# Kernel tuning notes

Measured on AMD Instinct MI355X. Metric: run time of the kernel, lower is better.

Reference implementation:

```python
import jax, jax.numpy as jnp
import numpy as np

B, S, D = 2, 2048, 1024
H, KVH, HD = 16, 1, 64
E, K, HID = 8, 2, 4096
EPS = 1e-5


def rmsnorm(x, scale):
    ms = jnp.mean(x * x, axis=-1, keepdims=True)
    return x * jax.lax.rsqrt(ms + EPS) * scale


def setup_inputs() -> dict:
    key = jax.random.key(0)
    ks = jax.random.split(key, 12)
    s = lambda k, shape, fan: jax.random.normal(k, shape, jnp.float32) * (fan ** -0.5)
    return {
        "x": jax.random.normal(ks[0], (B, S, D), jnp.float32),
        "g_pre_mqa": jnp.ones((D,), jnp.float32),
        "g_post_mqa": jnp.ones((D,), jnp.float32),
        "g_pre_moe": jnp.ones((D,), jnp.float32),
        "g_post_moe": jnp.ones((D,), jnp.float32),
        "Wq": s(ks[1], (D, H * HD), D),
        "Wk": s(ks[2], (D, KVH * HD), D),
        "Wv": s(ks[3], (D, KVH * HD), D),
        "Wo": s(ks[4], (H * HD, D), H * HD),
        "Wg": s(ks[5], (D, E), D),
        "We1": s(ks[6], (E, D, HID), D),
        "We2": s(ks[7], (E, HID, D), HID),
    }


def mqa(x, Wq, Wk, Wv, Wo):
    b, s, _ = x.shape
    q = (x @ Wq).reshape(b, s, H, HD).transpose(0, 2, 1, 3)     # [B,H,S,hd]
    k = (x @ Wk).reshape(b, s, KVH, HD).transpose(0, 2, 1, 3)   # [B,1,S,hd]
    v = (x @ Wv).reshape(b, s, KVH, HD).transpose(0, 2, 1, 3)
    scores = jnp.einsum('bhqd,bhkd->bhqk', q, jnp.broadcast_to(k, (b, H, s, HD))) / np.sqrt(HD)
    probs = jax.nn.softmax(scores, axis=-1)  # note: no causal mask, matching _standard_attention
    out = jnp.einsum('bhqk,bhkd->bhqd', probs, jnp.broadcast_to(v, (b, H, s, HD)))
    out = out.transpose(0, 2, 1, 3).reshape(b, s, H * HD)
    return out @ Wo


def moe(h, Wg, We1, We2):
    logits = h @ Wg                       # [B,S,E]
    probs = jax.nn.softmax(logits, axis=-1)
    topv, topi = jax.lax.top_k(probs, K)  # [B,S,K]
    # scatter top-k probs into full expert vector (non-chosen experts -> 0)
    routing = jnp.sum(jax.nn.one_hot(topi, E, dtype=h.dtype) * topv[..., None], axis=-2)  # [B,S,E]
    mid = jax.nn.gelu(jnp.einsum('bsd,edh->bseh', h, We1))
    eo = jnp.einsum('bseh,ehd->bsed', mid, We2)
    out = jnp.einsum('bse,bsed->bsd', routing, eo)
    return out, probs


def reference(x, g_pre_mqa, g_post_mqa, g_pre_moe, g_post_moe, Wq, Wk, Wv, Wo, Wg, We1, We2):
    # inference path: dropout and router noise disabled (training=False)
    x = x + rmsnorm(mqa(rmsnorm(x, g_pre_mqa), Wq, Wk, Wv, Wo), g_post_mqa)
    moe_out, routing_probs = moe(rmsnorm(x, g_pre_moe), Wg, We1, We2)
    x = x + rmsnorm(moe_out, g_post_moe)
    return x, routing_probs
```

## Files before the change

kernel.cpp:

```cpp
#include <hip/hip_runtime.h>
#include <hip/hip_bf16.h>
#include <math.h>

#define NTOK   4096
#define DMODEL 1024
#define SEQL   2048
#define QKVW   1152
#define NH     16
#define HDIM   64
#define NE     8
#define HIDD   4096
#define EPSV   1e-5f
#define KT     32

#define ASCL   256.f
#define WSCL   4096.f
#define OUTSCL (1.f/1048576.f)
#define SSCALE (0.125f/65536.f)
#define PBIAS  10.397207708399179f
#define DTHR   0.5f

typedef __attribute__((ext_vector_type(8))) short bf16x8;
typedef __attribute__((ext_vector_type(8))) _Float16 f16x8;
typedef __attribute__((ext_vector_type(4))) _Float16 f16x4;
typedef __attribute__((ext_vector_type(4))) float f32x4;

#define GLOBAL_AS __attribute__((address_space(1)))
#define LDS_AS    __attribute__((address_space(3)))
__device__ __forceinline__ void gl_lds16(const void* g, void* l){
  __builtin_amdgcn_global_load_lds((const GLOBAL_AS void*)g, (LDS_AS void*)l, 16u, 0, 0u);
}

__device__ __forceinline__ short f2b(float x){
  __hip_bfloat16 h = __float2bfloat16(x);
  return *reinterpret_cast<short*>(&h);
}
__device__ __forceinline__ void split2h(float x, _Float16& a, _Float16& b){
  a = (_Float16)x;
  b = (_Float16)(x - (float)a);
}

__global__ __launch_bounds__(256) void transpose_conv_kernel(
    const float* __restrict__ in, short* __restrict__ out,
    int R, int C, long inb, long outb)
{
  __shared__ float tile[32][33];
  in  += (size_t)blockIdx.z * inb;
  out += (size_t)blockIdx.z * outb;
  int c0 = blockIdx.x*32, r0 = blockIdx.y*32;
  int tx = threadIdx.x & 31, ty = threadIdx.x >> 5;
  #pragma unroll
  for (int i=0;i<4;i++)
    tile[ty+i*8][tx] = in[(size_t)(r0+ty+i*8)*C + c0+tx];
  __syncthreads();
  int cl = threadIdx.x >> 3, quad = threadIdx.x & 7;
  short4 s;
  s.x = f2b(tile[quad*4+0][cl]);
  s.y = f2b(tile[quad*4+1][cl]);
  s.z = f2b(tile[quad*4+2][cl]);
  s.w = f2b(tile[quad*4+3][cl]);
  *(short4*)&out[(size_t)(c0+cl)*R + r0 + quad*4] = s;
}

__global__ __launch_bounds__(256) void transpose_split2f16_kernel(
    const float* __restrict__ in, _Float16* __restrict__ o1, _Float16* __restrict__ o2,
    int R, int C, int rowOff, int outLD)
{
  __shared__ float tile[32][33];
  int c0 = blockIdx.x*32, r0 = blockIdx.y*32;
  int tx = threadIdx.x & 31, ty = threadIdx.x >> 5;
  #pragma unroll
  for (int i=0;i<4;i++)
    tile[ty+i*8][tx] = in[(size_t)(r0+ty+i*8)*C + c0+tx];
  __syncthreads();
  #pragma unroll
  for (int i=0;i<4;i++){
    float v = tile[tx][ty+i*8] * WSCL;
    _Float16 va,vb; split2h(v,va,vb);
    size_t idx = (size_t)(c0+ty+i*8+rowOff)*outLD + r0+tx;
    o1[idx]=va; o2[idx]=vb;
  }
}

__global__ __launch_bounds__(256) void rms_split2_kernel(
    const float* __restrict__ x, const float* __restrict__ g,
    _Float16* __restrict__ o1, _Float16* __restrict__ o2)
{
  int row = blockIdx.x, tid = threadIdx.x;
  const float4* xr = (const float4*)(x + (size_t)row*DMODEL);
  float4 v = xr[tid];
  float ss = v.x*v.x + v.y*v.y + v.z*v.z + v.w*v.w;
  #pragma unroll
  for (int off=32; off; off>>=1) ss += __shfl_down(ss, off);
  __shared__ float red[4];
  if ((tid&63)==0) red[tid>>6] = ss;
  __syncthreads();
  float rs = rsqrtf((red[0]+red[1]+red[2]+red[3])*(1.f/1024.f) + EPSV) * ASCL;
  float4 gv = ((const float4*)g)[tid];
  float o[4] = {v.x*rs*gv.x, v.y*rs*gv.y, v.z*rs*gv.z, v.w*rs*gv.w};
  f16x4 s1,s2;
  #pragma unroll
  for (int c=0;c<4;c++){ _Float16 a,b; split2h(o[c],a,b); s1[c]=a; s2[c]=b; }
  size_t base = (size_t)row*DMODEL + tid*4;
  *(f16x4*)(o1+base) = s1; *(f16x4*)(o2+base) = s2;
}

__global__ __launch_bounds__(256) void vtrans_split2_kernel(
    const _Float16* __restrict__ p1, const _Float16* __restrict__ p2,
    _Float16* __restrict__ o1, _Float16* __restrict__ o2)
{
  __shared__ float tile[32][33];
  int s0 = blockIdx.x*32, d0 = blockIdx.y*32, bb = blockIdx.z;
  int tx = threadIdx.x & 31, ty = threadIdx.x >> 5;
  #pragma unroll
  for (int i=0;i<4;i++){
    size_t idx = (size_t)(bb*SEQL + s0+ty+i*8)*QKVW + DMODEL+HDIM + d0+tx;
    tile[ty+i*8][tx] = (float)p1[idx] + (float)p2[idx];
  }
  __syncthreads();
  #pragma unroll
  for (int i=0;i<4;i++){
    float v = tile[tx][ty+i*8];
    _Float16 va,vb; split2h(v,va,vb);
    size_t idx = (size_t)(bb*HDIM + d0+ty+i*8)*SEQL + s0+tx;
    o1[idx]=va; o2[idx]=vb;
  }
}

__global__ __launch_bounds__(256) void gemm_f16x2_kernel(
    const _Float16* __restrict__ a1, const _Float16* __restrict__ a2,
    const _Float16* __restrict__ b1, const _Float16* __restrict__ b2,
    float* __restrict__ C, int K, int ldc, float outscale)
{
  __shared__ _Float16 lsA[2][128*32];
  __shared__ _Float16 lsB[2][128*32];
  int m0 = blockIdx.y*128, n0 = blockIdx.x*128;
  int tid = threadIdx.x, wave = tid>>6, lane = tid&63;
  int g = lane>>4, li = lane&15;
  int wm = (wave>>1)*64, wn = (wave&1)*64;
  const _Float16* Ap[2] = {a1,a2};
  const _Float16* Bp[2] = {b1,b2};
  int srow = wave*32 + (lane>>2), scol = (lane&3)*8;
  const _Float16* gA[2][2]; const _Float16* gB[2][2];
  #pragma unroll
  for (int p=0;p<2;p++)
    #pragma unroll
    for (int i=0;i<2;i++){
      gA[p][i] = Ap[p] + (size_t)(m0+srow+i*16)*K + scol;
      gB[p][i] = Bp[p] + (size_t)(n0+srow+i*16)*K + scol;
    }
  f32x4 acc[4][4] = {};
  for (int k0=0; k0<K; k0+=32){
    #pragma unroll
    for (int p=0;p<2;p++)
      #pragma unroll
      for (int i=0;i<2;i++){
        gl_lds16(gA[p][i]+k0, &lsA[p][(wave*32+i*16)*32]);
        gl_lds16(gB[p][i]+k0, &lsB[p][(wave*32+i*16)*32]);
      }
    __syncthreads();
    #pragma unroll
    for (int i=0;i<2;i++){
      f16x8 af[4];
      #pragma unroll
      for (int m=0;m<4;m++) af[m] = *(f16x8*)&lsA[i][(wm+m*16+li)*32 + g*8];
      #pragma unroll
      for (int j=0;j<2-i;j++){
        #pragma unroll
        for (int n=0;n<4;n++){
          f16x8 bfr = *(f16x8*)&lsB[j][(wn+n*16+li)*32 + g*8];
          #pragma unroll
          for (int m=0;m<4;m++)
            acc[m][n] = __builtin_amdgcn_mfma_f32_16x16x32_f16(af[m], bfr, acc[m][n], 0,0,0);
        }
      }
    }
    __syncthreads();
  }
  #pragma unroll
  for (int m=0;m<4;m++){
    int lr0 = wm + m*16 + g*4;
    #pragma unroll
    for (int n=0;n<4;n++){
      int col = n0 + wn + n*16 + li;
      #pragma unroll
      for (int r=0;r<4;r++)
        C[(size_t)(m0+lr0+r)*ldc + col] = acc[m][n][r]*outscale;
    }
  }
}

__global__ __launch_bounds__(256) void gemm_f16x2s_kernel(
    const _Float16* __restrict__ a1, const _Float16* __restrict__ a2,
    const _Float16* __restrict__ b1, const _Float16* __restrict__ b2,
    _Float16* __restrict__ o1, _Float16* __restrict__ o2, int K, int ldc, float outscale)
{
  __shared__ _Float16 lsA[2][128*32];
  __shared__ _Float16 lsB[2][128*32];
  int m0 = blockIdx.y*128, n0 = blockIdx.x*128;
  int tid = threadIdx.x, wave = tid>>6, lane = tid&63;
  int g = lane>>4, li = lane&15;
  int wm = (wave>>1)*64, wn = (wave&1)*64;
  const _Float16* Ap[2] = {a1,a2};
  const _Float16* Bp[2] = {b1,b2};
  int srow = wave*32 + (lane>>2), scol = (lane&3)*8;
  const _Float16* gA[2][2]; const _Float16* gB[2][2];
  #pragma unroll
  for (int p=0;p<2;p++)
    #pragma unroll
    for (int i=0;i<2;i++){
      gA[p][i] = Ap[p] + (size_t)(m0+srow+i*16)*K + scol;
      gB[p][i] = Bp[p] + (size_t)(n0+srow+i*16)*K + scol;
    }
  f32x4 acc[4][4] = {};
  for (int k0=0; k0<K; k0+=32){
    #pragma unroll
    for (int p=0;p<2;p++)
      #pragma unroll
      for (int i=0;i<2;i++){
        gl_lds16(gA[p][i]+k0, &lsA[p][(wave*32+i*16)*32]);
        gl_lds16(gB[p][i]+k0, &lsB[p][(wave*32+i*16)*32]);
      }
    __syncthreads();
    #pragma unroll
    for (int i=0;i<2;i++){
      f16x8 af[4];
      #pragma unroll
      for (int m=0;m<4;m++) af[m] = *(f16x8*)&lsA[i][(wm+m*16+li)*32 + g*8];
      #pragma unroll
      for (int j=0;j<2-i;j++){
        #pragma unroll
        for (int n=0;n<4;n++){
          f16x8 bfr = *(f16x8*)&lsB[j][(wn+n*16+li)*32 + g*8];
          #pragma unroll
          for (int m=0;m<4;m++)
            acc[m][n] = __builtin_amdgcn_mfma_f32_16x16x32_f16(af[m], bfr, acc[m][n], 0,0,0);
        }
      }
    }
    __syncthreads();
  }
  #pragma unroll
  for (int m=0;m<4;m++){
    int lr0 = wm + m*16 + g*4;
    #pragma unroll
    for (int n=0;n<4;n++){
      int col = n0 + wn + n*16 + li;
      #pragma unroll
      for (int r=0;r<4;r++){
        float val = acc[m][n][r]*outscale;
        _Float16 xa,xb; split2h(val,xa,xb);
        size_t idx = (size_t)(m0+lr0+r)*ldc + col;
        o1[idx]=xa; o2[idx]=xb;
      }
    }
  }
}

__global__ __launch_bounds__(256) void attn_f16_kernel(
    const _Float16* __restrict__ q1, const _Float16* __restrict__ q2,
    const _Float16* __restrict__ v1, const _Float16* __restrict__ v2,
    _Float16* __restrict__ o1, _Float16* __restrict__ o2)
{
  __shared__ _Float16 Ks[32*136];
  __shared__ _Float16 Vs[64*72];
  int qt = blockIdx.x, h = blockIdx.y, b = blockIdx.z;
  int tid = threadIdx.x, wave = tid>>6, lane = tid&63;
  int g = lane>>4, li = lane&15;
  size_t qbase = (size_t)b*SEQL + qt*128;
  const _Float16* qsrc[2] = {q1,q2};
  const _Float16* vsrc[2] = {v1,v2};
  f16x8 qf[2][2][2];
  #pragma unroll
  for (int nf=0;nf<2;nf++){
    size_t qrow = qbase + wave*32 + nf*16 + li;
    #pragma unroll
    for (int j=0;j<2;j++)
      #pragma unroll
      for (int kk=0;kk<2;kk++)
        qf[nf][j][kk] = *(const f16x8*)(qsrc[j] + qrow*QKVW + h*HDIM + kk*32 + g*8);
  }
  const _Float16* kga[2]; int klds[2];
  const _Float16* vga[2]; int vlds[2];
  #pragma unroll
  for (int i=0;i<2;i++){
    int c = tid + 256*i;
    { int row=c>>4, sub=c&15, pl=sub>>3, d=(sub&7)*8;
      kga[i] = qsrc[pl] + ((size_t)b*SEQL + row)*QKVW + DMODEL + d;
      klds[i] = row*136 + pl*64 + d; }
    { int row=c>>3, sub=c&7, pl=sub>>2, s8=(sub&3)*8;
      vga[i] = vsrc[pl] + ((size_t)b*HDIM + row)*SEQL + s8;
      vlds[i] = row*72 + pl*32 + s8; }
  }
  f16x8 kreg[2], vreg[2];
  #pragma unroll
  for (int i=0;i<2;i++){ kreg[i]=*(const f16x8*)kga[i]; vreg[i]=*(const f16x8*)vga[i]; }

  float m_run[2] = {-1e30f,-1e30f}, l_run[2] = {0.f,0.f};
  f32x4 acc_o[4][2] = {};
  int src1 = (((2*g)&3)<<4) + li;
  int src2 = (((2*g+1)&3)<<4) + li;
  bool hi_half = (g>=2);

  for (int kvt=0; kvt<SEQL/KT; kvt++){
    #pragma unroll
    for (int i=0;i<2;i++){
      *(f16x8*)&Ks[klds[i]] = kreg[i];
      *(f16x8*)&Vs[vlds[i]] = vreg[i];
    }
    __syncthreads();
    if (kvt+1 < SEQL/KT){
      #pragma unroll
      for (int i=0;i<2;i++){
        kreg[i] = *(const f16x8*)(kga[i] + (size_t)(kvt+1)*KT*QKVW);
        vreg[i] = *(const f16x8*)(vga[i] + (size_t)(kvt+1)*KT);
      }
    }
    f32x4 s_acc[2][2] = {};
    __builtin_amdgcn_s_setprio(1);
    #pragma unroll
    for (int i=0;i<2;i++){
      #pragma unroll
      for (int kk=0;kk<2;kk++){
        f16x8 af[2];
        #pragma unroll
        for (int mf=0;mf<2;mf++)
          af[mf] = *(f16x8*)&Ks[(mf*16+li)*136 + i*64 + kk*32 + g*8];
        #pragma unroll
        for (int j=0;j<2-i;j++){
          #pragma unroll
          for (int nf=0;nf<2;nf++){
            #pragma unroll
            for (int mf=0;mf<2;mf++)
              s_acc[mf][nf] = __builtin_amdgcn_mfma_f32_16x16x32_f16(af[mf], qf[nf][j][kk], s_acc[mf][nf], 0,0,0);
          }
        }
      }
    }
    __builtin_amdgcn_s_setprio(0);
    float p[2][2][4];
    #pragma unroll
    for (int nf=0;nf<2;nf++){
      float mx = -1e30f;
      #pragma unroll
      for (int mf=0;mf<2;mf++)
        #pragma unroll
        for (int r=0;r<4;r++) mx = fmaxf(mx, s_acc[mf][nf][r]);
      mx = fmaxf(mx, __shfl_xor(mx,16));
      mx = fmaxf(mx, __shfl_xor(mx,32));
      mx *= SSCALE;
      if (!__all(mx <= m_run[nf] + DTHR)){
        float mn = fmaxf(m_run[nf], mx);
        float al = __expf(m_run[nf] - mn);
        m_run[nf] = mn;
        l_run[nf] *= al;
        #pragma unroll
        for (int mfd=0; mfd<4; mfd++){
          acc_o[mfd][nf][0]*=al; acc_o[mfd][nf][1]*=al;
          acc_o[mfd][nf][2]*=al; acc_o[mfd][nf][3]*=al;
        }
      }
      float rsum = 0.f;
      #pragma unroll
      for (int mf=0;mf<2;mf++)
        #pragma unroll
        for (int r=0;r<4;r++){
          float pv = __expf(s_acc[mf][nf][r]*SSCALE - m_run[nf] + PBIAS);
          p[mf][nf][r] = pv; rsum += pv;
        }
      rsum += __shfl_xor(rsum,16);
      rsum += __shfl_xor(rsum,32);
      l_run[nf] += rsum;
    }
    f16x8 fp_frag[2][2];
    #pragma unroll
    for (int nf=0;nf<2;nf++){
      float p8[8];
      #pragma unroll
      for (int jj=0;jj<4;jj++){
        float v0 = __shfl(p[0][nf][jj], src1);
        float vv1 = __shfl(p[1][nf][jj], src1);
        p8[jj] = hi_half ? vv1 : v0;
        float w0 = __shfl(p[0][nf][jj], src2);
        float w1 = __shfl(p[1][nf][jj], src2);
        p8[4+jj] = hi_half ? w1 : w0;
      }
      #pragma unroll
      for (int jj=0;jj<8;jj++){
        _Float16 xa,xb; split2h(p8[jj], xa,xb);
        fp_frag[nf][0][jj]=xa; fp_frag[nf][1][jj]=xb;
      }
    }
    __builtin_amdgcn_s_setprio(1);
    #pragma unroll
    for (int vj=0;vj<2;vj++){
      f16x8 av[4];
      #pragma unroll
      for (int mfd=0;mfd<4;mfd++)
        av[mfd] = *(f16x8*)&Vs[(mfd*16+li)*72 + vj*32 + g*8];
      #pragma unroll
      for (int pi=0; pi<2-vj; pi++)
        #pragma unroll
        for (int mfd=0;mfd<4;mfd++)
          #pragma unroll
          for (int nf=0;nf<2;nf++)
            acc_o[mfd][nf] = __builtin_amdgcn_mfma_f32_16x16x32_f16(av[mfd], fp_frag[nf][pi], acc_o[mfd][nf], 0,0,0);
    }
    __builtin_amdgcn_s_setprio(0);
    __syncthreads();
  }
  #pragma unroll
  for (int nf=0;nf<2;nf++){
    float inv = 1.f/l_run[nf];
    size_t q = qbase + wave*32 + nf*16 + li;
    #pragma unroll
    for (int mfd=0;mfd<4;mfd++){
      int d0 = mfd*16 + g*4;
      f16x4 sa,sb;
      #pragma unroll
      for (int r=0;r<4;r++){
        _Float16 xa,xb; split2h(acc_o[mfd][nf][r]*inv, xa,xb);
        sa[r]=xa; sb[r]=xb;
      }
      size_t base = q*DMODEL + h*HDIM + d0;
      *(f16x4*)(o1+base)=sa; *(f16x4*)(o2+base)=sb;
    }
  }
}

__global__ __launch_bounds__(256) void attnres_router_kernel(
    const float* __restrict__ x, const float* __restrict__ ao,
    const float* __restrict__ gpost, const float* __restrict__ gpre,
    const float* __restrict__ Wg,
    float* __restrict__ x2, short* __restrict__ h,
    float* __restrict__ probs_out, int* __restrict__ tok_list,
    float* __restrict__ w_list, int* __restrict__ counts)
{
  int row = blockIdx.x, tid = threadIdx.x;
  float4 a  = ((const float4*)(ao + (size_t)row*DMODEL))[tid];
  float4 xv = ((const float4*)(x  + (size_t)row*DMODEL))[tid];
  float ss = a.x*a.x + a.y*a.y + a.z*a.z + a.w*a.w;
  #pragma unroll
  for (int off=32; off; off>>=1) ss += __shfl_down(ss, off);
  __shared__ float red[4];
  if ((tid&63)==0) red[tid>>6] = ss;
  __syncthreads();
  float rs1 = rsqrtf((red[0]+red[1]+red[2]+red[3])*(1.f/1024.f) + EPSV);
  float4 gp = ((const float4*)gpost)[tid];
  float4 o;
  o.x = xv.x + a.x*rs1*gp.x; o.y = xv.y + a.y*rs1*gp.y;
  o.z = xv.z + a.z*rs1*gp.z; o.w = xv.w + a.w*rs1*gp.w;
  ((float4*)(x2 + (size_t)row*DMODEL))[tid] = o;
  float s2 = o.x*o.x + o.y*o.y + o.z*o.z + o.w*o.w;
  __syncthreads();
  #pragma unroll
  for (int off=32; off; off>>=1) s2 += __shfl_down(s2, off);
  if ((tid&63)==0) red[tid>>6] = s2;
  __syncthreads();
  float rs2 = rsqrtf((red[0]+red[1]+red[2]+red[3])*(1.f/1024.f) + EPSV);
  float4 gm = ((const float4*)gpre)[tid];
  float n0 = o.x*rs2*gm.x, n1 = o.y*rs2*gm.y, n2 = o.z*rs2*gm.z, n3 = o.w*rs2*gm.w;
  short4 hs;
  hs.x = f2b(n0); hs.y = f2b(n1); hs.z = f2b(n2); hs.w = f2b(n3);
  *(short4*)(h + (size_t)row*DMODEL + tid*4) = hs;
  const float* wr = Wg + (size_t)(tid*4)*NE;
  float le[8];
  #pragma unroll
  for (int e=0;e<8;e++)
    le[e] = n0*wr[e] + n1*wr[NE+e] + n2*wr[2*NE+e] + n3*wr[3*NE+e];
  #pragma unroll
  for (int e=0;e<8;e++)
    #pragma unroll
    for (int off=32; off; off>>=1) le[e] += __shfl_xor(le[e], off);
  __shared__ float redl[4][8];
  if ((tid&63)==0)
    #pragma unroll
    for (int e=0;e<8;e++) redl[tid>>6][e] = le[e];
  __syncthreads();
  if (tid == 0){
    float l[8];
    #pragma unroll
    for (int e=0;e<8;e++) l[e] = redl[0][e]+redl[1][e]+redl[2][e]+redl[3][e];
    float mx = l[0];
    #pragma unroll
    for (int e=1;e<8;e++) mx = fmaxf(mx, l[e]);
    float pp[8], s = 0.f;
    #pragma unroll
    for (int e=0;e<8;e++){ pp[e] = expf(l[e]-mx); s += pp[e]; }
    float inv = 1.f/s;
    #pragma unroll
    for (int e=0;e<8;e++){ pp[e] *= inv; probs_out[(size_t)row*NE + e] = pp[e]; }
    int i1 = 0;
    #pragma unroll
    for (int e=1;e<8;e++) if (pp[e] > pp[i1]) i1 = e;
    int i2 = (i1==0) ? 1 : 0;
    #pragma unroll
    for (int e=0;e<8;e++) if (e != i1 && pp[e] > pp[i2]) i2 = e;
    int pos = atomicAdd(&counts[i1], 1);
    tok_list[i1*NTOK+pos] = row;
    w_list[i1*NTOK+pos] = pp[i1];
    pos = atomicAdd(&counts[i2], 1);
    tok_list[i2*NTOK+pos] = row | (1<<16);
    w_list[i2*NTOK+pos] = pp[i2];
  }
}

__global__ __launch_bounds__(256) void moe_gemm1_kernel(
    const short* __restrict__ h, const short* __restrict__ we1t,
    const int* __restrict__ tok_list, const int* __restrict__ counts,
    short* __restrict__ mid)
{
  int e = blockIdx.z;
  int cnt = counts[e];
  int m0 = blockIdx.y*128, n0 = blockIdx.x*128;
  if (m0 >= cnt) return;
  int base = 0;
  for (int j=0;j<NE;j++){ int c = counts[j]; if (j<e) base += c; }
  const short* Bt = we1t + (size_t)e*HIDD*DMODEL;
  const int* tl = tok_list + e*NTOK;
  __shared__ short lsA[128*32];
  __shared__ short lsB[128*32];
  int tid = threadIdx.x, wave = tid>>6, lane = tid&63;
  int li = lane&15, g = lane>>4;
  int wm = (wave>>1)*64, wn = (wave&1)*64;
  int srow = wave*32 + (lane>>2), scol = (lane&3)*8;
  const short* gA[2]; const short* gB[2];
  #pragma unroll
  for (int i=0;i<2;i++){
    int rr = min(m0+srow+i*16, cnt-1);
    gA[i] = h + (size_t)(tl[rr] & 0xFFFF)*DMODEL + scol;
    gB[i] = Bt + (size_t)(n0+srow+i*16)*DMODEL + scol;
  }
  f32x4 acc[4][4] = {};
  for (int k0=0; k0<DMODEL; k0+=32){
    #pragma unroll
    for (int i=0;i<2;i++){
      gl_lds16(gA[i]+k0, &lsA[(wave*32+i*16)*32]);
      gl_lds16(gB[i]+k0, &lsB[(wave*32+i*16)*32]);
    }
    __syncthreads();
    bf16x8 af[4], bfr[4];
    #pragma unroll
    for (int m=0;m<4;m++) af[m] = *(bf16x8*)&lsA[(wm+m*16+li)*32 + g*8];
    #pragma unroll
    for (int n=0;n<4;n++) bfr[n] = *(bf16x8*)&lsB[(wn+n*16+li)*32 + g*8];
    #pragma unroll
    for (int m=0;m<4;m++)
      #pragma unroll
      for (int n=0;n<4;n++)
        acc[m][n] = __builtin_amdgcn_mfma_f32_16x16x32_bf16(af[m], bfr[n], acc[m][n], 0,0,0);
    __syncthreads();
  }
  #pragma unroll
  for (int m=0;m<4;m++){
    int lr0 = wm + m*16 + (g<<2);
    #pragma unroll
    for (int n=0;n<4;n++){
      int col = n0 + wn + n*16 + li;
      #pragma unroll
      for (int r=0;r<4;r++){
        int gr = m0 + lr0 + r;
        if (gr < cnt){
          float tval = acc[m][n][r];
          float u = 1.5957691216057308f*(tval + 0.044715f*tval*tval*tval);
          float ge = tval / (1.f + __expf(-u));
          mid[(size_t)(base+gr)*HIDD + col] = f2b(ge);
        }
      }
    }
  }
}

__global__ __launch_bounds__(256) void moe_gemm2_kernel(
    const short* __restrict__ mid, const short* __restrict__ we2t,
    const int* __restrict__ tok_list, const float* __restrict__ w_list,
    const int* __restrict__ counts, float* __restrict__ eo)
{
  int e = blockIdx.z;
  int cnt = counts[e];
  int m0 = blockIdx.y*128, n0 = blockIdx.x*128;
  if (m0 >= cnt) return;
  int base = 0;
  for (int j=0;j<NE;j++){ int c = counts[j]; if (j<e) base += c; }
  const short* A  = mid + (size_t)base*HIDD;
  const short* Bt = we2t + (size_t)e*DMODEL*HIDD;
  const int* tl = tok_list + e*NTOK;
  const float* wl = w_list + e*NTOK;
  __shared__ short lsA[128*32];
  __shared__ short lsB[128*32];
  int tid = threadIdx.x, wave = tid>>6, lane = tid&63;
  int li = lane&15, g = lane>>4;
  int wm = (wave>>1)*64, wn = (wave&1)*64;
  int srow = wave*32 + (lane>>2), scol = (lane&3)*8;
  const short* gA[2]; const short* gB[2];
  #pragma unroll
  for (int i=0;i<2;i++){
    int rr = min(m0+srow+i*16, cnt-1);
    gA[i] = A + (size_t)rr*HIDD + scol;
    gB[i] = Bt + (size_t)(n0+srow+i*16)*HIDD + scol;
  }
  f32x4 acc[4][4] = {};
  for (int k0=0; k0<HIDD; k0+=32){
    #pragma unroll
    for (int i=0;i<2;i++){
      gl_lds16(gA[i]+k0, &lsA[(wave*32+i*16)*32]);
      gl_lds16(gB[i]+k0, &lsB[(wave*32+i*16)*32]);
    }
    __syncthreads();
    bf16x8 af[4], bfr[4];
    #pragma unroll
    for (int m=0;m<4;m++) af[m] = *(bf16x8*)&lsA[(wm+m*16+li)*32 + g*8];
    #pragma unroll
    for (int n=0;n<4;n++) bfr[n] = *(bf16x8*)&lsB[(wn+n*16+li)*32 + g*8];
    #pragma unroll
    for (int m=0;m<4;m++)
      #pragma unroll
      for (int n=0;n<4;n++)
        acc[m][n] = __builtin_amdgcn_mfma_f32_16x16x32_bf16(af[m], bfr[n], acc[m][n], 0,0,0);
    __syncthreads();
  }
  #pragma unroll
  for (int m=0;m<4;m++){
    int lr0 = wm + m*16 + (g<<2);
    #pragma unroll
    for (int n=0;n<4;n++){
      int col = n0 + wn + n*16 + li;
      #pragma unroll
      for (int r=0;r<4;r++){
        int gr = m0 + lr0 + r;
        if (gr < cnt){
          int pv = tl[gr];
          eo[((size_t)(pv>>16)*NTOK + (pv & 0xFFFF))*DMODEL + col] = wl[gr]*acc[m][n][r];
        }
      }
    }
  }
}

__global__ __launch_bounds__(256) void final_kernel(
    const float* __restrict__ x2, const float* __restrict__ eo,
    const float* __restrict__ g, float* __restrict__ out)
{
  int row = blockIdx.x, tid = threadIdx.x;
  float4 m0 = ((const float4*)(eo + (size_t)row*DMODEL))[tid];
  float4 m1 = ((const float4*)(eo + (size_t)(NTOK+row)*DMODEL))[tid];
  float4 mv;
  mv.x = m0.x+m1.x; mv.y = m0.y+m1.y; mv.z = m0.z+m1.z; mv.w = m0.w+m1.w;
  float4 xv = ((const float4*)(x2  + (size_t)row*DMODEL))[tid];
  float ss = mv.x*mv.x + mv.y*mv.y + mv.z*mv.z + mv.w*mv.w;
  #pragma unroll
  for (int off=32; off; off>>=1) ss += __shfl_down(ss, off);
  __shared__ float red[4];
  if ((tid&63)==0) red[tid>>6] = ss;
  __syncthreads();
  float rs = rsqrtf((red[0]+red[1]+red[2]+red[3])*(1.f/1024.f) + EPSV);
  float4 gv = ((const float4*)g)[tid];
  float4 o;
  o.x = xv.x + mv.x*rs*gv.x; o.y = xv.y + mv.y*rs*gv.y;
  o.z = xv.z + mv.z*rs*gv.z; o.w = xv.w + mv.w*rs*gv.w;
  ((float4*)(out + (size_t)row*DMODEL))[tid] = o;
}

extern "C" void kernel_launch(void* const* d_in, const int* in_sizes, int n_in,
                              void* d_out, int out_size, void* d_ws, size_t ws_size,
                              hipStream_t stream) {
  (void)in_sizes; (void)n_in; (void)out_size; (void)ws_size;
  const float* x          = (const float*)d_in[0];
  const float* g_pre_mqa  = (const float*)d_in[1];
  const float* g_post_mqa = (const float*)d_in[2];
  const float* g_pre_moe  = (const float*)d_in[3];
  const float* g_post_moe = (const float*)d_in[4];
  const float* Wq         = (const float*)d_in[5];
  const float* Wk         = (const float*)d_in[6];
  const float* Wv         = (const float*)d_in[7];
  const float* Wo         = (const float*)d_in[8];
  const float* Wg         = (const float*)d_in[9];
  const float* We1        = (const float*)d_in[10];
  const float* We2        = (const float*)d_in[11];

  float* out_x = (float*)d_out;
  float* out_probs = out_x + (size_t)NTOK*DMODEL;

  char* p = (char*)d_ws;
  size_t off = 0;
  auto alloc = [&](size_t bytes)->char*{
    char* r = p + off; off = (off + bytes + 255) & ~(size_t)255; return r; };

  short* we1t = (short*)alloc((size_t)NE*HIDD*DMODEL*2);
  short* we2t = (short*)alloc((size_t)NE*DMODEL*HIDD*2);
  short* mid  = (short*)alloc((size_t)2*NTOK*HIDD*2);

  char* regA = alloc((size_t)2*NTOK*DMODEL*2);
  _Float16* xn1p1 = (_Float16*)regA;
  _Float16* xn1p2 = (_Float16*)(regA + (size_t)NTOK*DMODEL*2);
  float* ao       = (float*)regA;

  _Float16* wqkvT1 = (_Float16*)alloc((size_t)QKVW*DMODEL*2);
  _Float16* wqkvT2 = (_Float16*)alloc((size_t)QKVW*DMODEL*2);
  _Float16* woT1   = (_Float16*)alloc((size_t)DMODEL*DMODEL*2);
  _Float16* woT2   = (_Float16*)alloc((size_t)DMODEL*DMODEL*2);

  char* regB = alloc((size_t)2*NTOK*DMODEL*2);
  _Float16* attnp1 = (_Float16*)regB;
  _Float16* attnp2 = (_Float16*)(regB + (size_t)NTOK*DMODEL*2);

  char* regC = alloc((size_t)2*NTOK*DMODEL*4 + (size_t)NTOK*DMODEL*2);
  _Float16* qkvf1 = (_Float16*)regC;
  _Float16* qkvf2 = (_Float16*)(regC + (size_t)NTOK*QKVW*2);
  float* eo    = (float*)regC;
  short* hbuf  = (short*)(regC + (size_t)2*NTOK*DMODEL*4);

  _Float16* vt1 = (_Float16*)alloc((size_t)2*HDIM*SEQL*2);
  _Float16* vt2 = (_Float16*)alloc((size_t)2*HDIM*SEQL*2);
  float* x2  = (float*)alloc((size_t)NTOK*DMODEL*4);
  int*   tok_l  = (int*)  alloc((size_t)NE*NTOK*4);
  float* w_l    = (float*)alloc((size_t)NE*NTOK*4);
  int*   counts = (int*)  alloc(256);

  transpose_conv_kernel<<<dim3(HIDD/32, DMODEL/32, NE), 256, 0, stream>>>(
      We1, we1t, DMODEL, HIDD, (long)DMODEL*HIDD, (long)HIDD*DMODEL);
  transpose_conv_kernel<<<dim3(DMODEL/32, HIDD/32, NE), 256, 0, stream>>>(
      We2, we2t, HIDD, DMODEL, (long)HIDD*DMODEL, (long)DMODEL*HIDD);
  transpose_split2f16_kernel<<<dim3(DMODEL/32, DMODEL/32), 256, 0, stream>>>(
      Wq, wqkvT1, wqkvT2, DMODEL, DMODEL, 0, DMODEL);
  transpose_split2f16_kernel<<<dim3(HDIM/32, DMODEL/32), 256, 0, stream>>>(
      Wk, wqkvT1, wqkvT2, DMODEL, HDIM, DMODEL, DMODEL);
  transpose_split2f16_kernel<<<dim3(HDIM/32, DMODEL/32), 256, 0, stream>>>(
      Wv, wqkvT1, wqkvT2, DMODEL, HDIM, DMODEL+HDIM, DMODEL);
  transpose_split2f16_kernel<<<dim3(DMODEL/32, DMODEL/32), 256, 0, stream>>>(
      Wo, woT1, woT2, DMODEL, DMODEL, 0, DMODEL);

  rms_split2_kernel<<<NTOK, 256, 0, stream>>>(x, g_pre_mqa, xn1p1, xn1p2);
  gemm_f16x2s_kernel<<<dim3(QKVW/128, NTOK/128), 256, 0, stream>>>(
      xn1p1, xn1p2, wqkvT1, wqkvT2, qkvf1, qkvf2, DMODEL, QKVW, OUTSCL*ASCL);
  vtrans_split2_kernel<<<dim3(SEQL/32, HDIM/32, 2), 256, 0, stream>>>(qkvf1, qkvf2, vt1, vt2);
  attn_f16_kernel<<<dim3(SEQL/128, NH, 2), 256, 0, stream>>>(
      qkvf1, qkvf2, vt1, vt2, attnp1, attnp2);
  gemm_f16x2_kernel<<<dim3(DMODEL/128, NTOK/128), 256, 0, stream>>>(
      attnp1, attnp2, woT1, woT2, ao, DMODEL, DMODEL, OUTSCL);

  hipMemsetAsync(counts, 0, 32, stream);
  attnres_router_kernel<<<NTOK, 256, 0, stream>>>(
      x, ao, g_post_mqa, g_pre_moe, Wg, x2, hbuf, out_probs, tok_l, w_l, counts);
  moe_gemm1_kernel<<<dim3(HIDD/128, NTOK/128, NE), 256, 0, stream>>>(
      hbuf, we1t, tok_l, counts, mid);
  moe_gemm2_kernel<<<dim3(DMODEL/128, NTOK/128, NE), 256, 0, stream>>>(
      mid, we2t, tok_l, w_l, counts, eo);
  final_kernel<<<NTOK, 256, 0, stream>>>(x2, eo, g_post_moe, out_x);
}
```

Baseline: 726.9 us.

## Split attention KV range across two blocks and merge with combine kernel

```diff
diff --git a/kernel.cpp b/kernel.cpp
--- a/kernel.cpp
+++ b/kernel.cpp
@@ -12,13 +12,14 @@
 #define HIDD   4096
 #define EPSV   1e-5f
 #define KT     32
+#define NKVT   (SEQL/KT)
 
 #define ASCL   256.f
 #define WSCL   4096.f
 #define OUTSCL (1.f/1048576.f)
-#define SSCALE (0.125f/65536.f)
-#define PBIAS  10.397207708399179f
-#define DTHR   0.5f
+#define SSCL2  (0.125f/65536.f*1.4426950408889634f)
+#define DTHRL2 0.7213475204444817f
+#define PB2    15.f
 
 typedef __attribute__((ext_vector_type(8))) short bf16x8;
 typedef __attribute__((ext_vector_type(8))) _Float16 f16x8;
@@ -260,11 +261,13 @@
 __global__ __launch_bounds__(256) void attn_f16_kernel(
     const _Float16* __restrict__ q1, const _Float16* __restrict__ q2,
     const _Float16* __restrict__ v1, const _Float16* __restrict__ v2,
-    _Float16* __restrict__ o1, _Float16* __restrict__ o2)
+    float* __restrict__ opart, float2* __restrict__ ml)
 {
   __shared__ _Float16 Ks[32*136];
   __shared__ _Float16 Vs[64*72];
-  int qt = blockIdx.x, h = blockIdx.y, b = blockIdx.z;
+  int qt = blockIdx.x, h = blockIdx.y, z = blockIdx.z;
+  int b = z>>1, kvh = z&1;
+  int kvstart = kvh*(NKVT/2), kvend = kvstart + NKVT/2;
   int tid = threadIdx.x, wave = tid>>6, lane = tid&63;
   int g = lane>>4, li = lane&15;
   size_t qbase = (size_t)b*SEQL + qt*128;
@@ -294,7 +297,10 @@
   }
   f16x8 kreg[2], vreg[2];
   #pragma unroll
-  for (int i=0;i<2;i++){ kreg[i]=*(const f16x8*)kga[i]; vreg[i]=*(const f16x8*)vga[i]; }
+  for (int i=0;i<2;i++){
+    kreg[i] = *(const f16x8*)(kga[i] + (size_t)kvstart*KT*QKVW);
+    vreg[i] = *(const f16x8*)(vga[i] + (size_t)kvstart*KT);
+  }
 
   float m_run[2] = {-1e30f,-1e30f}, l_run[2] = {0.f,0.f};
   f32x4 acc_o[4][2] = {};
@@ -302,14 +308,14 @@
   int src2 = (((2*g+1)&3)<<4) + li;
   bool hi_half = (g>=2);
 
-  for (int kvt=0; kvt<SEQL/KT; kvt++){
+  for (int kvt=kvstart; kvt<kvend; kvt++){
     #pragma unroll
     for (int i=0;i<2;i++){
       *(f16x8*)&Ks[klds[i]] = kreg[i];
       *(f16x8*)&Vs[vlds[i]] = vreg[i];
     }
     __syncthreads();
-    if (kvt+1 < SEQL/KT){
+    if (kvt+1 < kvend){
       #pragma unroll
       for (int i=0;i<2;i++){
         kreg[i] = *(const f16x8*)(kga[i] + (size_t)(kvt+1)*KT*QKVW);
@@ -348,10 +354,10 @@
         for (int r=0;r<4;r++) mx = fmaxf(mx, s_acc[mf][nf][r]);
       mx = fmaxf(mx, __shfl_xor(mx,16));
       mx = fmaxf(mx, __shfl_xor(mx,32));
-      mx *= SSCALE;
-      if (!__all(mx <= m_run[nf] + DTHR)){
+      mx *= SSCL2;
+      if (!__all(mx <= m_run[nf] + DTHRL2)){
         float mn = fmaxf(m_run[nf], mx);
-        float al = __expf(m_run[nf] - mn);
+        float al = exp2f(m_run[nf] - mn);
         m_run[nf] = mn;
         l_run[nf] *= al;
         #pragma unroll
@@ -361,11 +367,12 @@
         }
       }
       float rsum = 0.f;
+      float mb = m_run[nf] - PB2;
       #pragma unroll
       for (int mf=0;mf<2;mf++)
         #pragma unroll
         for (int r=0;r<4;r++){
-          float pv = __expf(s_acc[mf][nf][r]*SSCALE - m_run[nf] + PBIAS);
+          float pv = exp2f(s_acc[mf][nf][r]*SSCL2 - mb);
           p[mf][nf][r] = pv; rsum += pv;
         }
       rsum += __shfl_xor(rsum,16);
@@ -411,21 +418,43 @@
   }
   #pragma unroll
   for (int nf=0;nf<2;nf++){
-    float inv = 1.f/l_run[nf];
-    size_t q = qbase + wave*32 + nf*16 + li;
+    int ql = qt*128 + wave*32 + nf*16 + li;
+    size_t rowb = ((size_t)z*NH + h)*SEQL + ql;
     #pragma unroll
     for (int mfd=0;mfd<4;mfd++){
       int d0 = mfd*16 + g*4;
-      f16x4 sa,sb;
-      #pragma unroll
-      for (int r=0;r<4;r++){
-        _Float16 xa,xb; split2h(acc_o[mfd][nf][r]*inv, xa,xb);
-        sa[r]=xa; sb[r]=xb;
-      }
-      size_t base = q*DMODEL + h*HDIM + d0;
-      *(f16x4*)(o1+base)=sa; *(f16x4*)(o2+base)=sb;
-    }
-  }
+      float4 o4;
+      o4.x = acc_o[mfd][nf][0]; o4.y = acc_o[mfd][nf][1];
+      o4.z = acc_o[mfd][nf][2]; o4.w = acc_o[mfd][nf][3];
+      *(float4*)&opart[rowb*HDIM + d0] = o4;
+    }
+    if (g == 0) ml[rowb] = make_float2(m_run[nf], l_run[nf]);
+  }
+}
+
+__global__ __launch_bounds__(256) void attn_combine_kernel(
+    const float* __restrict__ opart, const float2* __restrict__ ml,
+    _Float16* __restrict__ o1, _Float16* __restrict__ o2)
+{
+  int row = blockIdx.x;
+  int b = row >> 11, ql = row & (SEQL-1);
+  int tid = threadIdx.x;
+  int h = tid >> 4, d0 = (tid & 15)*4;
+  size_t i0 = (((size_t)(b*2+0))*NH + h)*SEQL + ql;
+  size_t i1 = (((size_t)(b*2+1))*NH + h)*SEQL + ql;
+  float2 ml0 = ml[i0], ml1 = ml[i1];
+  float m = fmaxf(ml0.x, ml1.x);
+  float a0 = exp2f(ml0.x - m), a1 = exp2f(ml1.x - m);
+  float inv = 1.f/(ml0.y*a0 + ml1.y*a1);
+  float4 A0 = *(const float4*)&opart[i0*HDIM + d0];
+  float4 A1 = *(const float4*)&opart[i1*HDIM + d0];
+  float vals[4] = {(A0.x*a0+A1.x*a1)*inv, (A0.y*a0+A1.y*a1)*inv,
+                   (A0.z*a0+A1.z*a1)*inv, (A0.w*a0+A1.w*a1)*inv};
+  f16x4 s1,s2;
+  #pragma unroll
+  for (int c=0;c<4;c++){ _Float16 xa,xb; split2h(vals[c],xa,xb); s1[c]=xa; s2[c]=xb; }
+  size_t ob = (size_t)row*DMODEL + h*HDIM + d0;
+  *(f16x4*)(o1+ob)=s1; *(f16x4*)(o2+ob)=s2;
 }
 
 __global__ __launch_bounds__(256) void attnres_router_kernel(
@@ -689,6 +718,8 @@
   short* we1t = (short*)alloc((size_t)NE*HIDD*DMODEL*2);
   short* we2t = (short*)alloc((size_t)NE*DMODEL*HIDD*2);
   short* mid  = (short*)alloc((size_t)2*NTOK*HIDD*2);
+  float*  opart = (float*)mid;
+  float2* mlbuf = (float2*)((char*)mid + (size_t)4*NH*SEQL*HDIM*4);
 
   char* regA = alloc((size_t)2*NTOK*DMODEL*2);
   _Float16* xn1p1 = (_Float16*)regA;
@@ -734,8 +765,9 @@
   gemm_f16x2s_kernel<<<dim3(QKVW/128, NTOK/128), 256, 0, stream>>>(
       xn1p1, xn1p2, wqkvT1, wqkvT2, qkvf1, qkvf2, DMODEL, QKVW, OUTSCL*ASCL);
   vtrans_split2_kernel<<<dim3(SEQL/32, HDIM/32, 2), 256, 0, stream>>>(qkvf1, qkvf2, vt1, vt2);
-  attn_f16_kernel<<<dim3(SEQL/128, NH, 2), 256, 0, stream>>>(
-      qkvf1, qkvf2, vt1, vt2, attnp1, attnp2);
+  attn_f16_kernel<<<dim3(SEQL/128, NH, 4), 256, 0, stream>>>(
+      qkvf1, qkvf2, vt1, vt2, opart, mlbuf);
+  attn_combine_kernel<<<NTOK, 256, 0, stream>>>(opart, mlbuf, attnp1, attnp2);
   gemm_f16x2_kernel<<<dim3(DMODEL/128, NTOK/128), 256, 0, stream>>>(
       attnp1, attnp2, woT1, woT2, ao, DMODEL, DMODEL, OUTSCL);
 
```

New measurement: 743.8 us. 2.3% more time.
